# Optimization experiments

Hardware: AMD Instinct MI355X
Metric: run time of the kernel (lower is better)

Reference implementation:

```python
import jax, jax.numpy as jnp
import numpy as np

STATE_DIM = 1024
ACTION_DIM = 512
TASK_DIM = 64
EMBED = 64
HID = 128
B = 256


def setup_inputs() -> dict:
    key = jax.random.key(0)
    ks = jax.random.split(key, 24)
    s = 0.02
    inp = {
        "obs": jax.random.normal(ks[0], (B, STATE_DIM), dtype=jnp.float32),
        "task_label": jax.random.normal(ks[1], (B, TASK_DIM), dtype=jnp.float32),
        "action": jax.random.randint(ks[2], (B,), 0, ACTION_DIM, dtype=jnp.int64 if jax.config.jax_enable_x64 else jnp.int32),
        # task encoder: Linear(64,64) ReLU Linear(64,64) ReLU
        "we1": jax.random.normal(ks[3], (TASK_DIM, EMBED)) * s,
        "be1": jnp.zeros((EMBED,), jnp.float32),
        "we2": jax.random.normal(ks[4], (EMBED, EMBED)) * s,
        "be2": jnp.zeros((EMBED,), jnp.float32),
        # h_action net_W: Linear(64,128) ReLU Linear(128, 512*1024)
        "aw1": jax.random.normal(ks[5], (EMBED, HID)) * s,
        "aw1b": jnp.zeros((HID,), jnp.float32),
        "aw2": jax.random.normal(ks[6], (HID, ACTION_DIM * STATE_DIM)) * s,
        "aw2b": jnp.zeros((ACTION_DIM * STATE_DIM,), jnp.float32),
        # h_action net_b: Linear(64,128) ReLU Linear(128, 512)
        "ab1": jax.random.normal(ks[7], (EMBED, HID)) * s,
        "ab1b": jnp.zeros((HID,), jnp.float32),
        "ab2": jax.random.normal(ks[8], (HID, ACTION_DIM)) * s,
        "ab2b": jnp.zeros((ACTION_DIM,), jnp.float32),
        # h_critic net_W: Linear(64,128) ReLU Linear(128, 1*1024)
        "cw1": jax.random.normal(ks[9], (EMBED, HID)) * s,
        "cw1b": jnp.zeros((HID,), jnp.float32),
        "cw2": jax.random.normal(ks[10], (HID, 1 * STATE_DIM)) * s,
        "cw2b": jnp.zeros((STATE_DIM,), jnp.float32),
        # h_critic net_b: Linear(64,128) ReLU Linear(128, 1)
        "cb1": jax.random.normal(ks[11], (EMBED, HID)) * s,
        "cb1b": jnp.zeros((HID,), jnp.float32),
        "cb2": jax.random.normal(ks[12], (HID, 1)) * s,
        "cb2b": jnp.zeros((1,), jnp.float32),
    }
    return inp


def reference(obs, task_label, action, we1, be1, we2, be2,
              aw1, aw1b, aw2, aw2b, ab1, ab1b, ab2, ab2b,
              cw1, cw1b, cw2, cw2b, cb1, cb1b, cb2, cb2b):
    relu = jax.nn.relu
    b = obs.shape[0]
    # DummyBody: phi = phi_a = phi_v = obs
    # task encoder -> z [B, EMBED]
    z = relu(relu(task_label @ we1 + be1) @ we2 + be2)
    # hypernet-generated actor head: W [B, A, S], b [B, A]
    Wa = (relu(z @ aw1 + aw1b) @ aw2 + aw2b).reshape(b, ACTION_DIM, STATE_DIM)
    ba = relu(z @ ab1 + ab1b) @ ab2 + ab2b
    # hypernet-generated critic head: W [B, 1, S], b [B, 1]
    Wv = (relu(z @ cw1 + cw1b) @ cw2 + cw2b).reshape(b, 1, STATE_DIM)
    bv = relu(z @ cb1 + cb1b) @ cb2 + cb2b
    # bmm apply (torch.bmm(W, phi.unsqueeze(-1)).squeeze(-1) + b)
    logits = jnp.einsum('boi,bi->bo', Wa, obs) + ba
    v = jnp.einsum('boi,bi->bo', Wv, obs) + bv
    logp = jax.nn.log_softmax(logits, axis=-1)
    log_prob = jnp.take_along_axis(logp, action[:, None].astype(jnp.int32), axis=-1)  # [B,1]
    entropy = -jnp.sum(jnp.exp(logp) * logp, axis=-1, keepdims=True)  # [B,1]
    return logits, action, log_prob, entropy, v
```

## Files before the change

kernel.cpp:

```cpp
#include <hip/hip_runtime.h>
#include <hip/hip_bf16.h>

#define B_SZ 256
#define SDIM 1024
#define ADIM 512

#define BK 32
#define NSTEPS (SDIM / BK)
#define NBUF 4

typedef __attribute__((ext_vector_type(8))) short bf16x8;
typedef __attribute__((ext_vector_type(4))) float f32x4;

__device__ __forceinline__ unsigned short f2bf(float x) {
  union { float f; unsigned u; } v; v.f = x;
  unsigned r = v.u + 0x7FFFu + ((v.u >> 16) & 1u);
  return (unsigned short)(r >> 16);
}

__device__ __forceinline__ void gll16(const void* g, void* l) {
  __builtin_amdgcn_global_load_lds(
      (const __attribute__((address_space(1))) unsigned int*)g,
      (__attribute__((address_space(3))) unsigned int*)l, 16, 0, 0);
}

__device__ __forceinline__ unsigned cvtpk(float lo, float hi) {
  unsigned r;
  asm("v_cvt_pk_bf16_f32 %0, %1, %2" : "=v"(r) : "v"(lo), "v"(hi));
  return r;
}

__global__ __launch_bounds__(128) void kprep(
    const float* __restrict__ obs,
    const float* __restrict__ task, const int* __restrict__ action,
    const float* __restrict__ we1, const float* __restrict__ be1,
    const float* __restrict__ we2, const float* __restrict__ be2,
    const float* __restrict__ aw1, const float* __restrict__ aw1b,
    const float* __restrict__ ab1, const float* __restrict__ ab1b,
    const float* __restrict__ ab2, const float* __restrict__ ab2b,
    const float* __restrict__ cw1, const float* __restrict__ cw1b,
    const float* __restrict__ cb1, const float* __restrict__ cb1b,
    const float* __restrict__ cb2, const float* __restrict__ cb2b,
    const float* __restrict__ cw2b,
    float* __restrict__ ws_ha, float* __restrict__ ws_hc,
    unsigned short* __restrict__ ws_obs,
    float* __restrict__ out)
{
  const int b = blockIdx.x, t = threadIdx.x;
  __shared__ float s_task[64], s_t1[64], s_z[64], s_hb[128], s_red[128];

  float dotc = 0.0f;
  {
    const float4* orow = (const float4*)(obs + (size_t)b * SDIM);
    const float4* crow = (const float4*)cw2b;
    ushort4* wrow = (ushort4*)(ws_obs + (size_t)b * SDIM);
#pragma unroll
    for (int i = 0; i < 2; ++i) {
      const int idx = t + i * 128;
      float4 v = orow[idx];
      float4 w = crow[idx];
      dotc += v.x * w.x + v.y * w.y + v.z * w.z + v.w * w.w;
      ushort4 u;
      u.x = f2bf(v.x); u.y = f2bf(v.y); u.z = f2bf(v.z); u.w = f2bf(v.w);
      wrow[idx] = u;
    }
  }

  if (t < 64) s_task[t] = task[b * 64 + t];
  __syncthreads();
  if (t < 64) {
    float a = be1[t];
    for (int e = 0; e < 64; ++e) a += s_task[e] * we1[e * 64 + t];
    s_t1[t] = fmaxf(a, 0.0f);
  }
  __syncthreads();
  if (t < 64) {
    float a = be2[t];
    for (int e = 0; e < 64; ++e) a += s_t1[e] * we2[e * 64 + t];
    s_z[t] = fmaxf(a, 0.0f);
  }
  __syncthreads();
  {
    float a1 = aw1b[t], a2 = ab1b[t], a3 = cw1b[t], a4 = cb1b[t];
    for (int e = 0; e < 64; ++e) {
      const float zv = s_z[e];
      a1 += zv * aw1[e * 128 + t];
      a2 += zv * ab1[e * 128 + t];
      a3 += zv * cw1[e * 128 + t];
      a4 += zv * cb1[e * 128 + t];
    }
    ws_ha[b * 128 + t] = fmaxf(a1, 0.0f);
    s_hb[t] = fmaxf(a2, 0.0f);
    ws_hc[b * 128 + t] = fmaxf(a3, 0.0f);
    s_red[t] = fmaxf(a4, 0.0f) * cb2[t] + dotc;
  }
  __syncthreads();
  for (int o = t; o < ADIM; o += 128) {
    float a = ab2b[o];
    for (int h = 0; h < 128; ++h) a += s_hb[h] * ab2[h * ADIM + o];
    out[b * ADIM + o] = a;
  }
  for (int s = 64; s > 0; s >>= 1) {
    __syncthreads();
    if (t < s) s_red[t] += s_red[t + s];
  }
  if (t == 0) {
    out[131840 + b] = s_red[0] + cb2b[0];
    out[131072 + b] = (float)action[b];
  }
}

__global__ __launch_bounds__(512, 1) void khyper(
    const unsigned short* __restrict__ ws_obs,
    const float* __restrict__ aw2, const float* __restrict__ aw2b,
    const float* __restrict__ cw2,
    const float* __restrict__ ws_ha, const float* __restrict__ ws_hc,
    float* __restrict__ d_out)
{
  __shared__ float Wl[NBUF][128 * BK];
  __shared__ unsigned short Al[NBUF][256 * BK];

  const int tid = threadIdx.x;
  const int blk = blockIdx.x;

  int wtype;
  int o0 = 0;
  const float* Wbase;
  size_t wstride;
  if (blk < 512)      { wtype = 0; o0 = blk; Wbase = aw2 + (size_t)blk * SDIM; wstride = (size_t)ADIM * SDIM; }
  else if (blk < 516) { wtype = 1; o0 = (blk - 512) * 128; Wbase = aw2b + (size_t)o0 * SDIM; wstride = SDIM; }
  else                { wtype = 2; Wbase = cw2; wstride = SDIM; }

  const int wv = tid >> 6;
  const int lane = tid & 63;

  const float* wsrc[2];
  const unsigned short* asrc[2];
#pragma unroll
  for (int p = 0; p < 2; ++p) {
    const int sw = p * 512 + tid;
    const int n = sw >> 3, cs = sw & 7;
    wsrc[p] = Wbase + (size_t)n * wstride + ((cs ^ (n & 7)) << 2);
    const int b = sw >> 2, ca = sw & 3;
    asrc[p] = ws_obs + (size_t)b * SDIM + ((ca ^ (b & 3)) << 3);
  }

  auto STAGE = [&](int t) {
    const int buf = t & (NBUF - 1);
    const int k0 = t * BK;
    char* wb = (char*)(&Wl[buf][0]) + wv * 1024;
    char* ab = (char*)(&Al[buf][0]) + wv * 1024;
    gll16(wsrc[0] + k0, wb);
    gll16(wsrc[1] + k0, wb + 8192);
    gll16(asrc[0] + k0, ab);
    gll16(asrc[1] + k0, ab + 8192);
  };

  const int mbase = (wv & 3) * 64;
  const int nbaseL = (wv >> 2) * 64;
  const int lrow = lane & 15;
  const int grp = lane >> 4;

  int aoff[4];
#pragma unroll
  for (int mf = 0; mf < 4; ++mf) {
    const int b = mbase + mf * 16 + lrow;
    aoff[mf] = b * 64 + ((grp ^ (lrow & 3)) << 4);
  }
  int woff[4][2];
#pragma unroll
  for (int nf = 0; nf < 4; ++nf) {
    const int n = nbaseL + nf * 16 + lrow;
    woff[nf][0] = n * 128 + (((2 * grp) ^ (lrow & 7)) << 4);
    woff[nf][1] = n * 128 + (((2 * grp + 1) ^ (lrow & 7)) << 4);
  }

  f32x4 acc[4][4];
#pragma unroll
  for (int mf = 0; mf < 4; ++mf)
#pragma unroll
    for (int nf = 0; nf < 4; ++nf) acc[mf][nf] = (f32x4)(0.0f);

  auto COMPUTE = [&](int t) {
    const int buf = t & (NBUF - 1);
    const char* ab = (const char*)(&Al[buf][0]);
    const char* wb = (const char*)(&Wl[buf][0]);
    bf16x8 af[4];
#pragma unroll
    for (int mf = 0; mf < 4; ++mf)
      af[mf] = *(const bf16x8*)(ab + aoff[mf]);
    bf16x8 bfr[4];
#pragma unroll
    for (int nf = 0; nf < 4; ++nf) {
      float4 x = *(const float4*)(wb + woff[nf][0]);
      float4 y = *(const float4*)(wb + woff[nf][1]);
      union { bf16x8 v; unsigned u[4]; } q;
      q.u[0] = cvtpk(x.x, x.y);
      q.u[1] = cvtpk(x.z, x.w);
      q.u[2] = cvtpk(y.x, y.y);
      q.u[3] = cvtpk(y.z, y.w);
      bfr[nf] = q.v;
    }
#pragma unroll
    for (int mf = 0; mf < 4; ++mf)
#pragma unroll
      for (int nf = 0; nf < 4; ++nf)
        acc[mf][nf] = __builtin_amdgcn_mfma_f32_16x16x32_bf16(af[mf], bfr[nf], acc[mf][nf], 0, 0, 0);
  };

  STAGE(0); STAGE(1); STAGE(2); STAGE(3);
#pragma unroll 1
  for (int t = 0; t < NSTEPS; ++t) {
    if (t <= NSTEPS - 4)      asm volatile("s_waitcnt vmcnt(12)" ::: "memory");
    else if (t == NSTEPS - 3) asm volatile("s_waitcnt vmcnt(8)" ::: "memory");
    else if (t == NSTEPS - 2) asm volatile("s_waitcnt vmcnt(4)" ::: "memory");
    else                      asm volatile("s_waitcnt vmcnt(0)" ::: "memory");
    __builtin_amdgcn_s_barrier();
    __builtin_amdgcn_sched_barrier(0);
    COMPUTE(t);
    asm volatile("s_waitcnt lgkmcnt(0)" ::: "memory");
    __builtin_amdgcn_sched_barrier(0);
    __builtin_amdgcn_s_barrier();
    if (t + 4 < NSTEPS) STAGE(t + 4);
  }

  if (wtype == 1) {
#pragma unroll
    for (int mf = 0; mf < 4; ++mf) {
      const int b = mbase + mf * 16 + grp * 4;
#pragma unroll
      for (int nf = 0; nf < 4; ++nf) {
        const int col = o0 + nbaseL + nf * 16 + lrow;
#pragma unroll
        for (int r = 0; r < 4; ++r)
          atomicAdd(&d_out[(size_t)(b + r) * ADIM + col], acc[mf][nf][r]);
      }
    }
  } else {
    const float* haW = (wtype == 0) ? ws_ha : ws_hc;
    float val[4][4];
#pragma unroll
    for (int mf = 0; mf < 4; ++mf)
#pragma unroll
      for (int r = 0; r < 4; ++r) val[mf][r] = 0.0f;
#pragma unroll
    for (int nf = 0; nf < 4; ++nf) {
      const int hidx = nbaseL + nf * 16 + lrow;
#pragma unroll
      for (int mf = 0; mf < 4; ++mf) {
        const int b = mbase + mf * 16 + grp * 4;
#pragma unroll
        for (int r = 0; r < 4; ++r)
          val[mf][r] += haW[(size_t)(b + r) * 128 + hidx] * acc[mf][nf][r];
      }
    }
#pragma unroll
    for (int mf = 0; mf < 4; ++mf)
#pragma unroll
      for (int r = 0; r < 4; ++r) {
        float v = val[mf][r];
        v += __shfl_xor(v, 1, 64);
        v += __shfl_xor(v, 2, 64);
        v += __shfl_xor(v, 4, 64);
        v += __shfl_xor(v, 8, 64);
        val[mf][r] = v;
      }
    if (lrow == 0) {
#pragma unroll
      for (int mf = 0; mf < 4; ++mf) {
        const int b = mbase + mf * 16 + grp * 4;
#pragma unroll
        for (int r = 0; r < 4; ++r) {
          if (wtype == 0) atomicAdd(&d_out[(size_t)(b + r) * ADIM + o0], val[mf][r]);
          else            atomicAdd(&d_out[131840 + b + r], val[mf][r]);
        }
      }
    }
  }
}

__global__ __launch_bounds__(256) void kfinal(const int* __restrict__ action,
                                              float* __restrict__ d_out)
{
  const int b = blockIdx.x, t = threadIdx.x;
  const float* lrow = d_out + (size_t)b * ADIM;
  __shared__ float sM[4], sS[4], sT[4];

  const float x0 = lrow[t], x1 = lrow[t + 256];
  float m = fmaxf(x0, x1);
#pragma unroll
  for (int s = 1; s < 64; s <<= 1) m = fmaxf(m, __shfl_xor(m, s, 64));
  const int wv = t >> 6, ln = t & 63;
  if (ln == 0) sM[wv] = m;
  __syncthreads();
  m = fmaxf(fmaxf(sM[0], sM[1]), fmaxf(sM[2], sM[3]));

  const float d0 = x0 - m, d1 = x1 - m;
  const float e0 = expf(d0), e1 = expf(d1);
  float s1 = e0 + e1;
  float s2 = e0 * d0 + e1 * d1;
#pragma unroll
  for (int s = 1; s < 64; s <<= 1) {
    s1 += __shfl_xor(s1, s, 64);
    s2 += __shfl_xor(s2, s, 64);
  }
  if (ln == 0) { sS[wv] = s1; sT[wv] = s2; }
  __syncthreads();
  if (t == 0) {
    const float S = sS[0] + sS[1] + sS[2] + sS[3];
    const float T = sT[0] + sT[1] + sT[2] + sT[3];
    const float lnS = logf(S);
    const int a = action[b];
    d_out[131328 + b] = (lrow[a] - m) - lnS;
    d_out[131584 + b] = lnS - T / S;
  }
}

extern "C" void kernel_launch(void* const* d_in, const int* in_sizes, int n_in,
                              void* d_out_v, int out_size, void* d_ws, size_t ws_size,
                              hipStream_t stream) {
  const float* obs   = (const float*)d_in[0];
  const float* task  = (const float*)d_in[1];
  const int*   action= (const int*)  d_in[2];
  const float* we1   = (const float*)d_in[3];
  const float* be1   = (const float*)d_in[4];
  const float* we2   = (const float*)d_in[5];
  const float* be2   = (const float*)d_in[6];
  const float* aw1   = (const float*)d_in[7];
  const float* aw1b  = (const float*)d_in[8];
  const float* aw2   = (const float*)d_in[9];
  const float* aw2b  = (const float*)d_in[10];
  const float* ab1   = (const float*)d_in[11];
  const float* ab1b  = (const float*)d_in[12];
  const float* ab2   = (const float*)d_in[13];
  const float* ab2b  = (const float*)d_in[14];
  const float* cw1   = (const float*)d_in[15];
  const float* cw1b  = (const float*)d_in[16];
  const float* cw2   = (const float*)d_in[17];
  const float* cw2b  = (const float*)d_in[18];
  const float* cb1   = (const float*)d_in[19];
  const float* cb1b  = (const float*)d_in[20];
  const float* cb2   = (const float*)d_in[21];
  const float* cb2b  = (const float*)d_in[22];
  float* out = (float*)d_out_v;
  float* ws_ha = (float*)d_ws;
  float* ws_hc = ws_ha + 256 * 128;
  unsigned short* ws_obs = (unsigned short*)(ws_hc + 256 * 128);

  kprep<<<256, 128, 0, stream>>>(obs, task, action, we1, be1, we2, be2, aw1, aw1b,
                                 ab1, ab1b, ab2, ab2b, cw1, cw1b, cb1, cb1b,
                                 cb2, cb2b, cw2b, ws_ha, ws_hc, ws_obs, out);
  khyper<<<517, 512, 0, stream>>>(ws_obs, aw2, aw2b, cw2, ws_ha, ws_hc, out);
  kfinal<<<256, 256, 0, stream>>>(action, out);
}
```

Measured before the change: 183.9 us.

## Split hypernet GEMM into smaller N tiles with obs in pre-tiled global layout

After: 202.1 us. 9.9% more time.

```diff
diff --git a/kernel.cpp b/kernel.cpp
--- a/kernel.cpp
+++ b/kernel.cpp
@@ -5,9 +5,8 @@
 #define SDIM 1024
 #define ADIM 512
 
-#define BK 32
-#define NSTEPS (SDIM / BK)
-#define NBUF 4
+#define BKW 64
+#define NCH (SDIM / BKW)
 
 typedef __attribute__((ext_vector_type(8))) short bf16x8;
 typedef __attribute__((ext_vector_type(4))) float f32x4;
@@ -43,7 +42,7 @@
     const float* __restrict__ cb2, const float* __restrict__ cb2b,
     const float* __restrict__ cw2b,
     float* __restrict__ ws_ha, float* __restrict__ ws_hc,
-    unsigned short* __restrict__ ws_obs,
+    unsigned short* __restrict__ obsT,
     float* __restrict__ out)
 {
   const int b = blockIdx.x, t = threadIdx.x;
@@ -51,19 +50,18 @@
 
   float dotc = 0.0f;
   {
-    const float4* orow = (const float4*)(obs + (size_t)b * SDIM);
-    const float4* crow = (const float4*)cw2b;
-    ushort4* wrow = (ushort4*)(ws_obs + (size_t)b * SDIM);
-#pragma unroll
-    for (int i = 0; i < 2; ++i) {
-      const int idx = t + i * 128;
-      float4 v = orow[idx];
-      float4 w = crow[idx];
-      dotc += v.x * w.x + v.y * w.y + v.z * w.z + v.w * w.w;
-      ushort4 u;
-      u.x = f2bf(v.x); u.y = f2bf(v.y); u.z = f2bf(v.z); u.w = f2bf(v.w);
-      wrow[idx] = u;
-    }
+    const int kc = t >> 2, g = t & 3;
+    const float4* src = (const float4*)(obs + (size_t)b * SDIM + kc * 32 + g * 8);
+    const float4* cbp = (const float4*)(cw2b + kc * 32 + g * 8);
+    float4 x = src[0], y = src[1];
+    float4 c0 = cbp[0], c1 = cbp[1];
+    dotc = x.x * c0.x + x.y * c0.y + x.z * c0.z + x.w * c0.w
+         + y.x * c1.x + y.y * c1.y + y.z * c1.z + y.w * c1.w;
+    ushort4 u0, u1;
+    u0.x = f2bf(x.x); u0.y = f2bf(x.y); u0.z = f2bf(x.z); u0.w = f2bf(x.w);
+    u1.x = f2bf(y.x); u1.y = f2bf(y.y); u1.z = f2bf(y.z); u1.w = f2bf(y.w);
+    ushort4* d = (ushort4*)(obsT + ((size_t)(kc * 256 + b) * 4 + g) * 8);
+    d[0] = u0; d[1] = u1;
   }
 
   if (t < 64) s_task[t] = task[b * 64 + t];
@@ -110,169 +108,124 @@
   }
 }
 
-__global__ __launch_bounds__(512, 1) void khyper(
-    const unsigned short* __restrict__ ws_obs,
+__global__ __launch_bounds__(512, 8) void khyper(
+    const unsigned short* __restrict__ obsT,
     const float* __restrict__ aw2, const float* __restrict__ aw2b,
     const float* __restrict__ cw2,
     const float* __restrict__ ws_ha, const float* __restrict__ ws_hc,
     float* __restrict__ d_out)
 {
-  __shared__ float Wl[NBUF][128 * BK];
-  __shared__ unsigned short Al[NBUF][256 * BK];
+  __shared__ float Wl[2][32 * BKW];
 
   const int tid = threadIdx.x;
   const int blk = blockIdx.x;
 
-  int wtype;
-  int o0 = 0;
+  int wtype, o0 = 0, h0 = 0;
   const float* Wbase;
   size_t wstride;
-  if (blk < 512)      { wtype = 0; o0 = blk; Wbase = aw2 + (size_t)blk * SDIM; wstride = (size_t)ADIM * SDIM; }
-  else if (blk < 516) { wtype = 1; o0 = (blk - 512) * 128; Wbase = aw2b + (size_t)o0 * SDIM; wstride = SDIM; }
-  else                { wtype = 2; Wbase = cw2; wstride = SDIM; }
-
-  const int wv = tid >> 6;
-  const int lane = tid & 63;
-
-  const float* wsrc[2];
-  const unsigned short* asrc[2];
-#pragma unroll
-  for (int p = 0; p < 2; ++p) {
-    const int sw = p * 512 + tid;
-    const int n = sw >> 3, cs = sw & 7;
-    wsrc[p] = Wbase + (size_t)n * wstride + ((cs ^ (n & 7)) << 2);
-    const int b = sw >> 2, ca = sw & 3;
-    asrc[p] = ws_obs + (size_t)b * SDIM + ((ca ^ (b & 3)) << 3);
-  }
-
-  auto STAGE = [&](int t) {
-    const int buf = t & (NBUF - 1);
-    const int k0 = t * BK;
-    char* wb = (char*)(&Wl[buf][0]) + wv * 1024;
-    char* ab = (char*)(&Al[buf][0]) + wv * 1024;
-    gll16(wsrc[0] + k0, wb);
-    gll16(wsrc[1] + k0, wb + 8192);
-    gll16(asrc[0] + k0, ab);
-    gll16(asrc[1] + k0, ab + 8192);
+  if (blk < 2048) {
+    wtype = 0; o0 = blk >> 2; h0 = (blk & 3) * 32;
+    Wbase = aw2 + (size_t)h0 * ADIM * SDIM + (size_t)o0 * SDIM;
+    wstride = (size_t)ADIM * SDIM;
+  } else if (blk < 2064) {
+    wtype = 1; o0 = (blk - 2048) * 32;
+    Wbase = aw2b + (size_t)o0 * SDIM; wstride = SDIM;
+  } else {
+    wtype = 2; h0 = (blk - 2064) * 32;
+    Wbase = cw2 + (size_t)h0 * SDIM; wstride = SDIM;
+  }
+
+  const int srow = tid >> 4, sseg = tid & 15;
+  const float* wsrc = Wbase + (size_t)srow * wstride + ((sseg ^ (srow & 7)) << 2);
+  const int wv = tid >> 6, lane = tid & 63;
+  char* ldst = (char*)(&Wl[0][0]) + wv * 1024;
+
+  const int lrow = lane & 15, grp = lane >> 4;
+  const int mbase = (wv & 3) * 64;
+  const int nloc = (wv >> 2) * 16 + lrow;
+
+  const unsigned short* pA = obsT + ((size_t)(mbase + lrow) * 4 + grp) * 8;
+
+  int wb[2][2];
+#pragma unroll
+  for (int ks = 0; ks < 2; ++ks)
+#pragma unroll
+    for (int q = 0; q < 2; ++q)
+      wb[ks][q] = nloc * 256 + ((ks * 128 + grp * 32 + q * 16) ^ ((nloc & 7) << 4));
+
+  f32x4 acc[4];
+#pragma unroll
+  for (int mf = 0; mf < 4; ++mf) acc[mf] = (f32x4)(0.0f);
+
+  auto STAGE = [&](int c, int buf) {
+    gll16(wsrc + (size_t)c * BKW, ldst + buf * 8192);
   };
 
-  const int mbase = (wv & 3) * 64;
-  const int nbaseL = (wv >> 2) * 64;
-  const int lrow = lane & 15;
-  const int grp = lane >> 4;
-
-  int aoff[4];
-#pragma unroll
-  for (int mf = 0; mf < 4; ++mf) {
-    const int b = mbase + mf * 16 + lrow;
-    aoff[mf] = b * 64 + ((grp ^ (lrow & 3)) << 4);
-  }
-  int woff[4][2];
-#pragma unroll
-  for (int nf = 0; nf < 4; ++nf) {
-    const int n = nbaseL + nf * 16 + lrow;
-    woff[nf][0] = n * 128 + (((2 * grp) ^ (lrow & 7)) << 4);
-    woff[nf][1] = n * 128 + (((2 * grp + 1) ^ (lrow & 7)) << 4);
-  }
-
-  f32x4 acc[4][4];
-#pragma unroll
-  for (int mf = 0; mf < 4; ++mf)
-#pragma unroll
-    for (int nf = 0; nf < 4; ++nf) acc[mf][nf] = (f32x4)(0.0f);
-
-  auto COMPUTE = [&](int t) {
-    const int buf = t & (NBUF - 1);
-    const char* ab = (const char*)(&Al[buf][0]);
-    const char* wb = (const char*)(&Wl[buf][0]);
-    bf16x8 af[4];
-#pragma unroll
-    for (int mf = 0; mf < 4; ++mf)
-      af[mf] = *(const bf16x8*)(ab + aoff[mf]);
-    bf16x8 bfr[4];
-#pragma unroll
-    for (int nf = 0; nf < 4; ++nf) {
-      float4 x = *(const float4*)(wb + woff[nf][0]);
-      float4 y = *(const float4*)(wb + woff[nf][1]);
+  auto COMPUTE = [&](int buf) {
+    const char* wl = (const char*)(&Wl[0][0]) + buf * 8192;
+#pragma unroll
+    for (int ks = 0; ks < 2; ++ks) {
+      float4 x = *(const float4*)(wl + wb[ks][0]);
+      float4 y = *(const float4*)(wl + wb[ks][1]);
       union { bf16x8 v; unsigned u[4]; } q;
       q.u[0] = cvtpk(x.x, x.y);
       q.u[1] = cvtpk(x.z, x.w);
       q.u[2] = cvtpk(y.x, y.y);
       q.u[3] = cvtpk(y.z, y.w);
-      bfr[nf] = q.v;
+      bf16x8 a0 = *(const bf16x8*)(pA);
+      bf16x8 a1 = *(const bf16x8*)(pA + 512);
+      bf16x8 a2 = *(const bf16x8*)(pA + 1024);
+      bf16x8 a3 = *(const bf16x8*)(pA + 1536);
+      acc[0] = __builtin_amdgcn_mfma_f32_16x16x32_bf16(a0, q.v, acc[0], 0, 0, 0);
+      acc[1] = __builtin_amdgcn_mfma_f32_16x16x32_bf16(a1, q.v, acc[1], 0, 0, 0);
+      acc[2] = __builtin_amdgcn_mfma_f32_16x16x32_bf16(a2, q.v, acc[2], 0, 0, 0);
+      acc[3] = __builtin_amdgcn_mfma_f32_16x16x32_bf16(a3, q.v, acc[3], 0, 0, 0);
+      pA += 8192;
     }
-#pragma unroll
-    for (int mf = 0; mf < 4; ++mf)
-#pragma unroll
-      for (int nf = 0; nf < 4; ++nf)
-        acc[mf][nf] = __builtin_amdgcn_mfma_f32_16x16x32_bf16(af[mf], bfr[nf], acc[mf][nf], 0, 0, 0);
   };
 
-  STAGE(0); STAGE(1); STAGE(2); STAGE(3);
+  STAGE(0, 0);
+  __syncthreads();
 #pragma unroll 1
-  for (int t = 0; t < NSTEPS; ++t) {
-    if (t <= NSTEPS - 4)      asm volatile("s_waitcnt vmcnt(12)" ::: "memory");
-    else if (t == NSTEPS - 3) asm volatile("s_waitcnt vmcnt(8)" ::: "memory");
-    else if (t == NSTEPS - 2) asm volatile("s_waitcnt vmcnt(4)" ::: "memory");
-    else                      asm volatile("s_waitcnt vmcnt(0)" ::: "memory");
-    __builtin_amdgcn_s_barrier();
-    __builtin_amdgcn_sched_barrier(0);
-    COMPUTE(t);
-    asm volatile("s_waitcnt lgkmcnt(0)" ::: "memory");
-    __builtin_amdgcn_sched_barrier(0);
-    __builtin_amdgcn_s_barrier();
-    if (t + 4 < NSTEPS) STAGE(t + 4);
+  for (int c = 0; c < NCH; ++c) {
+    if (c + 1 < NCH) STAGE(c + 1, (c + 1) & 1);
+    COMPUTE(c & 1);
+    __syncthreads();
   }
 
   if (wtype == 1) {
+    const int o = o0 + nloc;
 #pragma unroll
     for (int mf = 0; mf < 4; ++mf) {
       const int b = mbase + mf * 16 + grp * 4;
 #pragma unroll
-      for (int nf = 0; nf < 4; ++nf) {
-        const int col = o0 + nbaseL + nf * 16 + lrow;
-#pragma unroll
-        for (int r = 0; r < 4; ++r)
-          atomicAdd(&d_out[(size_t)(b + r) * ADIM + col], acc[mf][nf][r]);
-      }
+      for (int r = 0; r < 4; ++r)
+        atomicAdd(&d_out[(size_t)(b + r) * ADIM + o], acc[mf][r]);
     }
   } else {
-    const float* haW = (wtype == 0) ? ws_ha : ws_hc;
-    float val[4][4];
-#pragma unroll
-    for (int mf = 0; mf < 4; ++mf)
-#pragma unroll
-      for (int r = 0; r < 4; ++r) val[mf][r] = 0.0f;
-#pragma unroll
-    for (int nf = 0; nf < 4; ++nf) {
-      const int hidx = nbaseL + nf * 16 + lrow;
-#pragma unroll
-      for (int mf = 0; mf < 4; ++mf) {
-        const int b = mbase + mf * 16 + grp * 4;
-#pragma unroll
-        for (int r = 0; r < 4; ++r)
-          val[mf][r] += haW[(size_t)(b + r) * 128 + hidx] * acc[mf][nf][r];
-      }
-    }
-#pragma unroll
-    for (int mf = 0; mf < 4; ++mf)
+    const float* hw = (wtype == 0) ? ws_ha : ws_hc;
+    const int h = h0 + nloc;
+#pragma unroll
+    for (int mf = 0; mf < 4; ++mf) {
+      const int b = mbase + mf * 16 + grp * 4;
+      float val[4];
+#pragma unroll
+      for (int r = 0; r < 4; ++r)
+        val[r] = hw[(size_t)(b + r) * 128 + h] * acc[mf][r];
 #pragma unroll
       for (int r = 0; r < 4; ++r) {
-        float v = val[mf][r];
+        float v = val[r];
         v += __shfl_xor(v, 1, 64);
         v += __shfl_xor(v, 2, 64);
         v += __shfl_xor(v, 4, 64);
         v += __shfl_xor(v, 8, 64);
-        val[mf][r] = v;
+        val[r] = v;
       }
-    if (lrow == 0) {
-#pragma unroll
-      for (int mf = 0; mf < 4; ++mf) {
-        const int b = mbase + mf * 16 + grp * 4;
+      if (lrow == 0) {
 #pragma unroll
         for (int r = 0; r < 4; ++r) {
-          if (wtype == 0) atomicAdd(&d_out[(size_t)(b + r) * ADIM + o0], val[mf][r]);
-          else            atomicAdd(&d_out[131840 + b + r], val[mf][r]);
+          if (wtype == 0) atomicAdd(&d_out[(size_t)(b + r) * ADIM + o0], val[r]);
+          else            atomicAdd(&d_out[131840 + b + r], val[r]);
         }
       }
     }
@@ -345,11 +298,11 @@
   float* out = (float*)d_out_v;
   float* ws_ha = (float*)d_ws;
   float* ws_hc = ws_ha + 256 * 128;
-  unsigned short* ws_obs = (unsigned short*)(ws_hc + 256 * 128);
+  unsigned short* obsT = (unsigned short*)(ws_hc + 256 * 128);
 
   kprep<<<256, 128, 0, stream>>>(obs, task, action, we1, be1, we2, be2, aw1, aw1b,
                                  ab1, ab1b, ab2, ab2b, cw1, cw1b, cb1, cb1b,
-                                 cb2, cb2b, cw2b, ws_ha, ws_hc, ws_obs, out);
-  khyper<<<517, 512, 0, stream>>>(ws_obs, aw2, aw2b, cw2, ws_ha, ws_hc, out);
+                                 cb2, cb2b, cw2b, ws_ha, ws_hc, obsT, out);
+  khyper<<<2068, 512, 0, stream>>>(obsT, aw2, aw2b, cw2, ws_ha, ws_hc, out);
   kfinal<<<256, 256, 0, stream>>>(action, out);
 }
```
